# Kernel optimization log

Hardware: AMD Instinct MI355X
Metric: run time of the kernel (lower is better)

Reference implementation:

```python
import jax, jax.numpy as jnp
import numpy as np

B, S, ENC2, DEC = 32, 4096, 1024, 512

def setup_inputs() -> dict:
    key = jax.random.key(0)
    k1, k2, k3 = jax.random.split(key, 3)
    hidden = jax.random.normal(k1, (B, DEC), dtype=jnp.float32)
    context = jax.random.normal(k2, (B, S, ENC2), dtype=jnp.float32)
    mask = jnp.ones((B, S), dtype=jnp.int32)
    # Linear(enc*2+dec -> dec): weight [DEC, ENC2+DEC], bias [DEC]
    W_attn = jax.random.normal(k3, (DEC, ENC2 + DEC), dtype=jnp.float32) * (1.0 / np.sqrt(ENC2 + DEC))
    b_attn = jnp.zeros((DEC,), dtype=jnp.float32)
    v = jax.random.uniform(jax.random.fold_in(key, 7), (DEC,), dtype=jnp.float32)
    return {"hidden": hidden, "context": context, "mask": mask,
            "W_attn": W_attn, "b_attn": b_attn, "v": v}

def reference(hidden, context, mask, W_attn, b_attn, v):
    # cat((hidden repeated over S, context)) @ W.T == hidden@Wh.T + context@Wc.T
    # split W to avoid materializing the [B,S,1536] concat
    Wh = W_attn[:, :DEC]          # acts on hidden (first in cat)
    Wc = W_attn[:, DEC:]          # acts on context
    h_proj = hidden @ Wh.T + b_attn                      # [B, DEC]
    c_proj = jnp.einsum('bse,de->bsd', context, Wc)      # [B, S, DEC]
    sim = jnp.tanh(h_proj[:, None, :] + c_proj)          # [B, S, DEC]
    scores = jnp.einsum('bsd,d->bs', sim, v)             # [B, S]
    scores = jnp.where(mask == 0, -jnp.inf, scores)
    return jax.nn.softmax(scores, axis=1)
```

## Files before the change

kernel.cpp:

```cpp
#include <hip/hip_runtime.h>
#include <hip/hip_bf16.h>
#include <cmath>

#define NB 32
#define NS 4096
#define NK 1024
#define ND 512
#define WSTRIDE 1536
#define NT 32

using bf16x8 = __attribute__((ext_vector_type(8))) __bf16;
using f32x4  = __attribute__((ext_vector_type(4))) float;
typedef unsigned short u16;

__device__ inline u16 f2b(float x) {
    __hip_bfloat16 h = __float2bfloat16(x);
    u16 u; __builtin_memcpy(&u, &h, 2); return u;
}

__device__ inline float fast_tanh(float x) {
    float xc = fminf(fmaxf(x, -10.f), 10.f);
    float e = __expf(2.f * xc);
    return (e - 1.f) / (e + 1.f);
}

__global__ void prep_kernel(const float* __restrict__ W, const float* __restrict__ hidden,
                            const float* __restrict__ bias, u16* __restrict__ wcb,
                            float* __restrict__ hp) {
    const int blk = blockIdx.x, tid = threadIdx.x;
    if (blk < 2048) {
        int idx = blk * 256 + tid;
        int R = idx >> 10, k = idx & 1023;
        float val = W[(size_t)R * WSTRIDE + ND + k];
        int ks = k >> 5, S = (k >> 3) & 3, j = k & 7;
        int g = (R << 2) + (S ^ ((R >> 1) & 3));
        wcb[(ks << 14) + (g << 3) + j] = f2b(val);
    } else {
        int g = blk - 2048;
        int b = g >> 1;
        int d = ((g & 1) << 8) + tid;
        __shared__ float sh[ND];
        sh[tid] = hidden[b * ND + tid];
        sh[256 + tid] = hidden[b * ND + 256 + tid];
        __syncthreads();
        const float4* wr = (const float4*)(W + (size_t)d * WSTRIDE);
        float acc = bias[d];
#pragma unroll 8
        for (int k = 0; k < ND / 4; k++) {
            float4 w4 = wr[k];
            acc += w4.x * sh[4 * k] + w4.y * sh[4 * k + 1] + w4.z * sh[4 * k + 2] + w4.w * sh[4 * k + 3];
        }
        hp[b * ND + d] = acc;
    }
}

__global__ __launch_bounds__(1024, 4)
void fused_scores_kernel(const float* __restrict__ ctx, const u16* __restrict__ wcb,
                         const float* __restrict__ hp, const float* __restrict__ vvec,
                         float* __restrict__ scores) {
    __shared__ __align__(16) char lA[2][128 * 64];
    __shared__ __align__(16) char lB[2][512 * 64];

    const int tid = threadIdx.x;
    const int blk = blockIdx.x;
    const int b  = blk >> 5;
    const int s0 = (blk & 31) << 7;

    const int lane = tid & 63, wid = tid >> 6;
    const int l15 = lane & 15, l4 = lane >> 4;
    const int wm = wid >> 3, wn = wid & 7;

    const int srow = tid >> 3, q = tid & 7;
    const float4* asrc = (const float4*)(ctx + (size_t)b * NS * NK + (size_t)(s0 + srow) * NK);
    const int awbyte = (srow << 6) + ((((q >> 1) ^ ((srow >> 1) & 3))) << 4) + ((q & 1) << 3);

    int aoff[4], boff[4];
#pragma unroll
    for (int r = 0; r < 4; r++) {
        int row = (wm << 6) + (r << 4) + l15;
        aoff[r] = (row << 6) + ((l4 ^ ((row >> 1) & 3)) << 4);
    }
#pragma unroll
    for (int c = 0; c < 4; c++) {
        int row = (wn << 6) + (c << 4) + l15;
        boff[c] = (row << 6) + ((l4 ^ ((row >> 1) & 3)) << 4);
    }

    f32x4 acc[4][4];
    f32x4 zero = {0.f, 0.f, 0.f, 0.f};
#pragma unroll
    for (int r = 0; r < 4; r++)
#pragma unroll
        for (int c = 0; c < 4; c++) acc[r][c] = zero;

    const char* wcb_bytes = (const char*)wcb;
    float4 va;

#define STAGE_B_DMA(chunk, buf)                                                      \
    _Pragma("unroll")                                                                \
    for (int i = 0; i < 2; i++) {                                                    \
        const char* src = wcb_bytes + ((size_t)(chunk) << 15)                        \
                          + (((((wid << 1) + i) << 6) + lane) << 4);                 \
        __builtin_amdgcn_global_load_lds(                                            \
            (const __attribute__((address_space(1))) void*)src,                      \
            (__attribute__((address_space(3))) void*)(&lB[buf][((wid << 1) + i) << 10]), \
            16, 0, 0);                                                               \
    }

#define CVT_WRITE_A(buf)                                                             \
    {                                                                                \
        ushort4 a4;                                                                  \
        a4.x = f2b(va.x); a4.y = f2b(va.y); a4.z = f2b(va.z); a4.w = f2b(va.w);      \
        *(ushort4*)(&lA[buf][awbyte]) = a4;                                          \
    }

#define MFMA_CLUSTER(abuf, bbuf)                                                     \
    {                                                                                \
        bf16x8 af[4], bfr[4];                                                        \
        _Pragma("unroll")                                                            \
        for (int r = 0; r < 4; r++) af[r] = *(const bf16x8*)(&lA[abuf][aoff[r]]);    \
        _Pragma("unroll")                                                            \
        for (int c = 0; c < 4; c++) bfr[c] = *(const bf16x8*)(&lB[bbuf][boff[c]]);   \
        asm volatile("s_waitcnt lgkmcnt(0)" ::: "memory");                           \
        __builtin_amdgcn_sched_barrier(0);                                           \
        __builtin_amdgcn_s_setprio(1);                                               \
        _Pragma("unroll")                                                            \
        for (int r = 0; r < 4; r++)                                                  \
            _Pragma("unroll")                                                        \
            for (int c = 0; c < 4; c++)                                              \
                acc[r][c] = __builtin_amdgcn_mfma_f32_16x16x32_bf16(                 \
                    af[r], bfr[c], acc[r][c], 0, 0, 0);                              \
        __builtin_amdgcn_s_setprio(0);                                               \
    }

    STAGE_B_DMA(0, 0);
    va = asrc[q];
    asm volatile("s_waitcnt vmcnt(0)" ::: "memory");
    CVT_WRITE_A(0);
    va = asrc[8 + q];
    asm volatile("s_waitcnt lgkmcnt(0)" ::: "memory");
    __builtin_amdgcn_s_barrier();
    __builtin_amdgcn_sched_barrier(0);

#pragma unroll 2
    for (int t = 0; t < NT; t++) {
        const int cur = t & 1, nxt = cur ^ 1;
        const int cB = (t + 1 < NT) ? t + 1 : NT - 1;
        const int tA = (t + 2 < NT) ? t + 2 : NT - 1;

        STAGE_B_DMA(cB, nxt);
        MFMA_CLUSTER(cur, cur);
        asm volatile("s_waitcnt vmcnt(2)" ::: "memory");
        CVT_WRITE_A(nxt);
        va = asrc[(tA << 3) + q];
        asm volatile("s_waitcnt vmcnt(1) lgkmcnt(0)" ::: "memory");
        __builtin_amdgcn_s_barrier();
        __builtin_amdgcn_sched_barrier(0);
    }

    const float* hpb = hp + b * ND;
    float part[4][4];
#pragma unroll
    for (int r = 0; r < 4; r++)
#pragma unroll
        for (int i = 0; i < 4; i++) part[r][i] = 0.f;

#pragma unroll
    for (int c = 0; c < 4; c++) {
        int d = (wn << 6) + (c << 4) + l15;
        float hpv = hpb[d], vv = vvec[d];
#pragma unroll
        for (int r = 0; r < 4; r++)
#pragma unroll
            for (int i = 0; i < 4; i++)
                part[r][i] += fast_tanh(acc[r][c][i] + hpv) * vv;
    }

    float* sc = (float*)lA;
#pragma unroll
    for (int r = 0; r < 4; r++) {
#pragma unroll
        for (int i = 0; i < 4; i++) {
            float p = part[r][i];
            p += __shfl_xor(p, 1); p += __shfl_xor(p, 2);
            p += __shfl_xor(p, 4); p += __shfl_xor(p, 8);
            if (l15 == 0) sc[(wn << 7) + (wm << 6) + (r << 4) + (l4 << 2) + i] = p;
        }
    }
    __syncthreads();
    if (tid < 128) {
        float s = 0.f;
#pragma unroll
        for (int w = 0; w < 8; w++) s += sc[(w << 7) + tid];
        scores[(size_t)b * NS + s0 + tid] = s;
    }
}

__global__ void softmax_kernel(const float* __restrict__ scores, const int* __restrict__ mask,
                               float* __restrict__ out) {
    int b = blockIdx.x, tid = threadIdx.x;
    __shared__ float red[256];
    float loc[16];
    float mx = -INFINITY;
#pragma unroll
    for (int i = 0; i < 16; i++) {
        int idx = i * 256 + tid;
        float s = scores[b * NS + idx];
        if (mask[b * NS + idx] == 0) s = -INFINITY;
        loc[i] = s;
        mx = fmaxf(mx, s);
    }
    red[tid] = mx; __syncthreads();
    for (int off = 128; off; off >>= 1) { if (tid < off) red[tid] = fmaxf(red[tid], red[tid + off]); __syncthreads(); }
    mx = red[0]; __syncthreads();
    float sum = 0.f;
#pragma unroll
    for (int i = 0; i < 16; i++) { float e = __expf(loc[i] - mx); loc[i] = e; sum += e; }
    red[tid] = sum; __syncthreads();
    for (int off = 128; off; off >>= 1) { if (tid < off) red[tid] += red[tid + off]; __syncthreads(); }
    float inv = 1.f / red[0];
#pragma unroll
    for (int i = 0; i < 16; i++) out[b * NS + i * 256 + tid] = loc[i] * inv;
}

extern "C" void kernel_launch(void* const* d_in, const int* in_sizes, int n_in,
                              void* d_out, int out_size, void* d_ws, size_t ws_size,
                              hipStream_t stream) {
    const float* hidden  = (const float*)d_in[0];
    const float* context = (const float*)d_in[1];
    const int*   mask    = (const int*)d_in[2];
    const float* W_attn  = (const float*)d_in[3];
    const float* b_attn  = (const float*)d_in[4];
    const float* v       = (const float*)d_in[5];
    float* out           = (float*)d_out;

    char* ws = (char*)d_ws;
    u16*   wcb    = (u16*)ws;
    float* hp     = (float*)(ws + (1 << 20));
    float* scores = (float*)(ws + (1 << 20) + (64 << 10));

    prep_kernel<<<2112, 256, 0, stream>>>(W_attn, hidden, b_attn, wcb, hp);
    fused_scores_kernel<<<NB * 32, 1024, 0, stream>>>(context, wcb, hp, v, scores);
    softmax_kernel<<<NB, 256, 0, stream>>>(scores, mask, out);
}
```

Before: 257.3 us.

## Halve block size to 512 threads with 4x8 MFMA tiles per wave and phased pipeline

Changes the fused GEMM block from 16 waves to 8 waves, so each wave computes a 64x128 output tile (4x8 MFMA accumulators) instead of 64x64. A-fragments are reused across more B columns. Each thread now loads two float4 of context and does twice the DMA for B. The K-step is split into four barrier-separated MFMA phases so the LDS reads and A conversion interleave with MFMAs. This raises register pressure (128 accumulator floats per lane) and adds more barriers per step.

```diff
diff --git a/kernel.cpp b/kernel.cpp
--- a/kernel.cpp
+++ b/kernel.cpp
@@ -10,6 +10,7 @@
 #define NT 32
 
 using bf16x8 = __attribute__((ext_vector_type(8))) __bf16;
+using u16x8  = __attribute__((ext_vector_type(8))) unsigned short;
 using f32x4  = __attribute__((ext_vector_type(4))) float;
 typedef unsigned short u16;
 
@@ -54,7 +55,7 @@
     }
 }
 
-__global__ __launch_bounds__(1024, 4)
+__global__ __launch_bounds__(512, 2)
 void fused_scores_kernel(const float* __restrict__ ctx, const u16* __restrict__ wcb,
                          const float* __restrict__ hp, const float* __restrict__ vvec,
                          float* __restrict__ scores) {
@@ -68,76 +69,76 @@
 
     const int lane = tid & 63, wid = tid >> 6;
     const int l15 = lane & 15, l4 = lane >> 4;
-    const int wm = wid >> 3, wn = wid & 7;
-
-    const int srow = tid >> 3, q = tid & 7;
+    const int wm = wid >> 2, wn = wid & 3;
+
+    const int srow = tid >> 2, q = tid & 3;
     const float4* asrc = (const float4*)(ctx + (size_t)b * NS * NK + (size_t)(s0 + srow) * NK);
-    const int awbyte = (srow << 6) + ((((q >> 1) ^ ((srow >> 1) & 3))) << 4) + ((q & 1) << 3);
-
-    int aoff[4], boff[4];
+    const int awbyte = (srow << 6) + ((q ^ ((srow >> 1) & 3)) << 4);
+
+    int aoff[4], boff[8];
 #pragma unroll
     for (int r = 0; r < 4; r++) {
         int row = (wm << 6) + (r << 4) + l15;
         aoff[r] = (row << 6) + ((l4 ^ ((row >> 1) & 3)) << 4);
     }
 #pragma unroll
-    for (int c = 0; c < 4; c++) {
-        int row = (wn << 6) + (c << 4) + l15;
+    for (int c = 0; c < 8; c++) {
+        int row = (wn << 7) + (c << 4) + l15;
         boff[c] = (row << 6) + ((l4 ^ ((row >> 1) & 3)) << 4);
     }
 
-    f32x4 acc[4][4];
+    f32x4 acc[4][8];
     f32x4 zero = {0.f, 0.f, 0.f, 0.f};
 #pragma unroll
     for (int r = 0; r < 4; r++)
 #pragma unroll
-        for (int c = 0; c < 4; c++) acc[r][c] = zero;
+        for (int c = 0; c < 8; c++) acc[r][c] = zero;
 
     const char* wcb_bytes = (const char*)wcb;
-    float4 va;
+    float4 va0, va1;
 
 #define STAGE_B_DMA(chunk, buf)                                                      \
     _Pragma("unroll")                                                                \
-    for (int i = 0; i < 2; i++) {                                                    \
+    for (int i = 0; i < 4; i++) {                                                    \
         const char* src = wcb_bytes + ((size_t)(chunk) << 15)                        \
-                          + (((((wid << 1) + i) << 6) + lane) << 4);                 \
+                          + (((((wid << 2) + i) << 6) + lane) << 4);                 \
         __builtin_amdgcn_global_load_lds(                                            \
             (const __attribute__((address_space(1))) void*)src,                      \
-            (__attribute__((address_space(3))) void*)(&lB[buf][((wid << 1) + i) << 10]), \
+            (__attribute__((address_space(3))) void*)(&lB[buf][((wid << 2) + i) << 10]), \
             16, 0, 0);                                                               \
     }
 
 #define CVT_WRITE_A(buf)                                                             \
     {                                                                                \
-        ushort4 a4;                                                                  \
-        a4.x = f2b(va.x); a4.y = f2b(va.y); a4.z = f2b(va.z); a4.w = f2b(va.w);      \
-        *(ushort4*)(&lA[buf][awbyte]) = a4;                                          \
-    }
-
-#define MFMA_CLUSTER(abuf, bbuf)                                                     \
+        u16x8 a8;                                                                    \
+        a8[0] = f2b(va0.x); a8[1] = f2b(va0.y); a8[2] = f2b(va0.z); a8[3] = f2b(va0.w); \
+        a8[4] = f2b(va1.x); a8[5] = f2b(va1.y); a8[6] = f2b(va1.z); a8[7] = f2b(va1.w); \
+        *(u16x8*)(&lA[buf][awbyte]) = a8;                                            \
+    }
+
+#define PHASE_MFMA(c0)                                                               \
     {                                                                                \
-        bf16x8 af[4], bfr[4];                                                        \
-        _Pragma("unroll")                                                            \
-        for (int r = 0; r < 4; r++) af[r] = *(const bf16x8*)(&lA[abuf][aoff[r]]);    \
-        _Pragma("unroll")                                                            \
-        for (int c = 0; c < 4; c++) bfr[c] = *(const bf16x8*)(&lB[bbuf][boff[c]]);   \
+        __builtin_amdgcn_s_barrier();                                                \
         asm volatile("s_waitcnt lgkmcnt(0)" ::: "memory");                           \
         __builtin_amdgcn_sched_barrier(0);                                           \
         __builtin_amdgcn_s_setprio(1);                                               \
         _Pragma("unroll")                                                            \
         for (int r = 0; r < 4; r++)                                                  \
-            _Pragma("unroll")                                                        \
-            for (int c = 0; c < 4; c++)                                              \
-                acc[r][c] = __builtin_amdgcn_mfma_f32_16x16x32_bf16(                 \
-                    af[r], bfr[c], acc[r][c], 0, 0, 0);                              \
+            acc[r][c0] = __builtin_amdgcn_mfma_f32_16x16x32_bf16(af[r], bA, acc[r][c0], 0, 0, 0); \
+        _Pragma("unroll")                                                            \
+        for (int r = 0; r < 4; r++)                                                  \
+            acc[r][c0 + 1] = __builtin_amdgcn_mfma_f32_16x16x32_bf16(af[r], bB, acc[r][c0 + 1], 0, 0, 0); \
         __builtin_amdgcn_s_setprio(0);                                               \
+        __builtin_amdgcn_s_barrier();                                                \
     }
 
     STAGE_B_DMA(0, 0);
-    va = asrc[q];
+    va0 = asrc[2 * q];
+    va1 = asrc[2 * q + 1];
     asm volatile("s_waitcnt vmcnt(0)" ::: "memory");
     CVT_WRITE_A(0);
-    va = asrc[8 + q];
+    va0 = asrc[8 + 2 * q];
+    va1 = asrc[8 + 2 * q + 1];
     asm volatile("s_waitcnt lgkmcnt(0)" ::: "memory");
     __builtin_amdgcn_s_barrier();
     __builtin_amdgcn_sched_barrier(0);
@@ -148,14 +149,36 @@
         const int cB = (t + 1 < NT) ? t + 1 : NT - 1;
         const int tA = (t + 2 < NT) ? t + 2 : NT - 1;
 
-        STAGE_B_DMA(cB, nxt);
-        MFMA_CLUSTER(cur, cur);
-        asm volatile("s_waitcnt vmcnt(2)" ::: "memory");
-        CVT_WRITE_A(nxt);
-        va = asrc[(tA << 3) + q];
-        asm volatile("s_waitcnt vmcnt(1) lgkmcnt(0)" ::: "memory");
-        __builtin_amdgcn_s_barrier();
-        __builtin_amdgcn_sched_barrier(0);
+        bf16x8 af[4];
+
+        {
+            STAGE_B_DMA(cB, nxt);
+#pragma unroll
+            for (int r = 0; r < 4; r++) af[r] = *(const bf16x8*)(&lA[cur][aoff[r]]);
+            bf16x8 bA = *(const bf16x8*)(&lB[cur][boff[0]]);
+            bf16x8 bB = *(const bf16x8*)(&lB[cur][boff[1]]);
+            PHASE_MFMA(0);
+        }
+        {
+            bf16x8 bA = *(const bf16x8*)(&lB[cur][boff[2]]);
+            bf16x8 bB = *(const bf16x8*)(&lB[cur][boff[3]]);
+            asm volatile("s_waitcnt vmcnt(4)" ::: "memory");
+            CVT_WRITE_A(nxt);
+            va0 = asrc[(tA << 3) + 2 * q];
+            va1 = asrc[(tA << 3) + 2 * q + 1];
+            PHASE_MFMA(2);
+        }
+        {
+            bf16x8 bA = *(const bf16x8*)(&lB[cur][boff[4]]);
+            bf16x8 bB = *(const bf16x8*)(&lB[cur][boff[5]]);
+            PHASE_MFMA(4);
+        }
+        {
+            bf16x8 bA = *(const bf16x8*)(&lB[cur][boff[6]]);
+            bf16x8 bB = *(const bf16x8*)(&lB[cur][boff[7]]);
+            asm volatile("s_waitcnt vmcnt(2)" ::: "memory");
+            PHASE_MFMA(6);
+        }
     }
 
     const float* hpb = hp + b * ND;
@@ -166,8 +189,8 @@
         for (int i = 0; i < 4; i++) part[r][i] = 0.f;
 
 #pragma unroll
-    for (int c = 0; c < 4; c++) {
-        int d = (wn << 6) + (c << 4) + l15;
+    for (int c = 0; c < 8; c++) {
+        int d = (wn << 7) + (c << 4) + l15;
         float hpv = hpb[d], vv = vvec[d];
 #pragma unroll
         for (int r = 0; r < 4; r++)
@@ -189,9 +212,7 @@
     }
     __syncthreads();
     if (tid < 128) {
-        float s = 0.f;
-#pragma unroll
-        for (int w = 0; w < 8; w++) s += sc[(w << 7) + tid];
+        float s = sc[tid] + sc[128 + tid] + sc[256 + tid] + sc[384 + tid];
         scores[(size_t)b * NS + s0 + tid] = s;
     }
 }
@@ -240,6 +261,6 @@
     float* scores = (float*)(ws + (1 << 20) + (64 << 10));
 
     prep_kernel<<<2112, 256, 0, stream>>>(W_attn, hidden, b_attn, wcb, hp);
-    fused_scores_kernel<<<NB * 32, 1024, 0, stream>>>(context, wcb, hp, v, scores);
+    fused_scores_kernel<<<NB * 32, 512, 0, stream>>>(context, wcb, hp, v, scores);
     softmax_kernel<<<NB, 256, 0, stream>>>(scores, mask, out);
 }
```

Result: slower. 305.1 us (+18.6%).
